# Optimization experiments

Hardware: AMD Instinct MI355X
Metric: run time of the kernel (lower is better)

Reference implementation:

```python
import jax, jax.numpy as jnp
import numpy as np

B, T, E, H = 4, 1024, 1024, 16
D = E // H  # head_dim = 64


def setup_inputs() -> dict:
    key = jax.random.key(0)
    ks = jax.random.split(key, 6)
    s = 0.02  # realistic init scale for stable softmax
    return {
        "hidden_states": jax.random.normal(ks[0], (B, T, E), jnp.float32),
        "attention_mask": jnp.zeros((B, 1, T, T), jnp.float32),
        "Wq": jax.random.normal(ks[1], (E, E), jnp.float32) * s,
        "bq": jnp.zeros((E,), jnp.float32),
        "Wk": jax.random.normal(ks[2], (E, E), jnp.float32) * s,
        "bk": jnp.zeros((E,), jnp.float32),
        "Wv": jax.random.normal(ks[3], (E, E), jnp.float32) * s,
        "bv": jnp.zeros((E,), jnp.float32),
        "Wo": jax.random.normal(ks[4], (E, E), jnp.float32) * s,
        "bo": jnp.zeros((E,), jnp.float32),
    }


def reference(hidden_states, attention_mask, Wq, bq, Wk, bk, Wv, bv, Wo, bo):
    b, t, e = hidden_states.shape
    scaling = jnp.asarray(D, hidden_states.dtype) ** -0.5
    # q_proj weights/bias are pre-scaled in the module; equivalent to scaling q output
    q = (hidden_states @ Wq.T + bq) * scaling      # [B,T,E]
    k = hidden_states @ Wk.T + bk                   # self-attention path (no cache)
    v = hidden_states @ Wv.T + bv
    q = q.reshape(b, t, H, D)
    k = k.reshape(b, t, H, D)
    v = v.reshape(b, t, H, D)
    # bmm(q, k^T): [B,H,T,S] score matrix (materialized, as in the original)
    scores = jnp.einsum("bthd,bshd->bhts", q, k) + attention_mask
    probs = jax.nn.softmax(scores, axis=-1)
    ctx = jnp.einsum("bhts,bshd->bthd", probs, v).reshape(b, t, e)
    return ctx @ Wo.T + bo
```

## Files before the change

kernel.cpp:

```cpp
#include <hip/hip_runtime.h>
#include <math.h>

#define BB 4
#define TT 1024
#define EE 1024
#define HH 16
#define DD 64
#define KDIM 1024
#define N_HS (4096 * 1024)
#define N_W  (1024 * 1024)
#define NQKV (BB * HH * TT * DD)
#define NMASK (BB * TT * TT)

typedef _Float16 f16x8 __attribute__((ext_vector_type(8)));
typedef _Float16 f16x4 __attribute__((ext_vector_type(4)));
typedef float    f32x4 __attribute__((ext_vector_type(4)));

__device__ __forceinline__ unsigned short f2h(float x) {
    _Float16 h = (_Float16)x;
    return __builtin_bit_cast(unsigned short, h);
}
__device__ __forceinline__ void split_h(float x, unsigned short& hi, unsigned short& lo) {
    _Float16 h = (_Float16)x;
    hi = __builtin_bit_cast(unsigned short, h);
    lo = f2h(x - (float)h);
}

__device__ __forceinline__ void gload16(const void* g, void* l) {
    __builtin_amdgcn_global_load_lds(
        (const __attribute__((address_space(1))) void*)g,
        (__attribute__((address_space(3))) void*)l, 16, 0, 0);
}

__global__ __launch_bounds__(256)
void split_kernel(const float* __restrict__ hs,
                  const float* __restrict__ Wq, const float* __restrict__ Wk,
                  const float* __restrict__ Wv, const float* __restrict__ Wo,
                  const float* __restrict__ maskp,
                  unsigned short* __restrict__ ws,
                  unsigned short* __restrict__ maskh)
{
    const int u = blockIdx.x * 256 + threadIdx.x;
    const float* src;
    unsigned short* dst;
    if (u < (N_HS / 4)) {
        src = hs + (size_t)u * 4;
        dst = ws + (size_t)u * 4;
    } else if (u < (N_HS / 4) + N_W) {
        int v = u - N_HS / 4;
        int wsel = v >> 18;
        int wo   = v & 0x3FFFF;
        const float* Wsrc = (wsel == 0) ? Wq : (wsel == 1) ? Wk : (wsel == 2) ? Wv : Wo;
        src = Wsrc + (size_t)wo * 4;
        dst = ws + (size_t)N_HS + (size_t)wsel * N_W + (size_t)wo * 4;
    } else {
        int v = u - (N_HS / 4) - N_W;
        src = maskp + (size_t)v * 4;
        dst = maskh + (size_t)v * 4;
    }
    float4 x = *(const float4*)src;
    ushort4 h4;
    h4.x = f2h(x.x); h4.y = f2h(x.y); h4.z = f2h(x.z); h4.w = f2h(x.w);
    *(ushort4*)dst = h4;
}

__global__ __launch_bounds__(256)
void qkv_kernel(const unsigned short* __restrict__ hsp,
                const unsigned short* __restrict__ wqp,
                const float* __restrict__ bq, const float* __restrict__ bk,
                const float* __restrict__ bv,
                unsigned short* __restrict__ qkvb)
{
    __shared__ unsigned short Ah[128 * 32], Bh[128 * 32];

    const int widx  = blockIdx.x >> 3;
    const int nbase = (blockIdx.x & 7) * 128;
    const int mbase = blockIdx.y * 128;
    const unsigned short* Wp = wqp + (size_t)widx * N_W;
    const float* bias = (widx == 0) ? bq : (widx == 1) ? bk : bv;
    unsigned short* dst = qkvb + (size_t)widx * NQKV;
    const float scale = (widx == 0) ? 0.125f : 1.0f;

    const int tid  = threadIdx.x;
    const int w    = tid >> 6;
    const int lane = tid & 63;
    const int quad = lane >> 4;
    const int l16  = lane & 15;
    const int wm   = (w >> 1) * 64;
    const int wn   = (w & 1) * 64;

    f32x4 acc[4][4];
#pragma unroll
    for (int i = 0; i < 4; i++)
#pragma unroll
        for (int j = 0; j < 4; j++) acc[i][j] = (f32x4)0.f;

#pragma unroll 1
    for (int kt = 0; kt < KDIM; kt += 32) {
        __syncthreads();
#pragma unroll
        for (int i = 0; i < 2; i++) {
            int u = tid + i * 256;
            int r = u >> 2, c = u & 3;
            int q = c ^ ((r >> 1) & 3);
            gload16(hsp + (size_t)(mbase + r) * KDIM + kt + q * 8, &Ah[u * 8]);
            gload16(Wp  + (size_t)(nbase + r) * KDIM + kt + q * 8, &Bh[u * 8]);
        }
        __syncthreads();

        f16x8 af[4], bfr[4];
#pragma unroll
        for (int i = 0; i < 4; i++) {
            int r = wm + i * 16 + l16;
            af[i] = *(const f16x8*)&Ah[(r * 4 + (quad ^ ((r >> 1) & 3))) * 8];
        }
#pragma unroll
        for (int j = 0; j < 4; j++) {
            int r = wn + j * 16 + l16;
            bfr[j] = *(const f16x8*)&Bh[(r * 4 + (quad ^ ((r >> 1) & 3))) * 8];
        }
#pragma unroll
        for (int i = 0; i < 4; i++)
#pragma unroll
            for (int j = 0; j < 4; j++)
                acc[i][j] = __builtin_amdgcn_mfma_f32_16x16x32_f16(af[i], bfr[j], acc[i][j], 0, 0, 0);
    }

#pragma unroll
    for (int j = 0; j < 4; j++) {
        int n = nbase + wn + j * 16 + l16;
        int h = n >> 6, d = n & 63;
        float bj = bias[n];
#pragma unroll
        for (int i = 0; i < 4; i++)
#pragma unroll
            for (int rr = 0; rr < 4; rr++) {
                int m = mbase + wm + i * 16 + quad * 4 + rr;
                int b = m >> 10, t = m & 1023;
                dst[(((size_t)(b * HH + h) * TT + t) * DD + d)] =
                    f2h((acc[i][j][rr] + bj) * scale);
            }
    }
}

__global__ __launch_bounds__(256)
void vtrans_kernel(const unsigned short* __restrict__ vp,
                   unsigned short* __restrict__ vtp)
{
    __shared__ unsigned short Ts[64 * 72];
    const int bh = blockIdx.y;
    const int t0 = blockIdx.x * 64;
    const unsigned short* src = vp  + (size_t)bh * TT * DD + (size_t)t0 * DD;
    unsigned short*       dst = vtp + (size_t)bh * DD * TT + t0;
    const int tid = threadIdx.x;

#pragma unroll
    for (int i = 0; i < 2; i++) {
        int id = tid + i * 256;
        int r = id >> 3, c = id & 7;
        *(uint4*)&Ts[r * 72 + c * 8] = *(const uint4*)(src + (size_t)r * DD + c * 8);
    }
    __syncthreads();
#pragma unroll
    for (int i = 0; i < 2; i++) {
        int id = tid + i * 256;
        int d = id >> 3, c = id & 7;
        unsigned short tmp[8];
#pragma unroll
        for (int j = 0; j < 8; j++) tmp[j] = Ts[(c * 8 + j) * 72 + d];
        uint4 o;
        o.x = (unsigned int)tmp[0] | ((unsigned int)tmp[1] << 16);
        o.y = (unsigned int)tmp[2] | ((unsigned int)tmp[3] << 16);
        o.z = (unsigned int)tmp[4] | ((unsigned int)tmp[5] << 16);
        o.w = (unsigned int)tmp[6] | ((unsigned int)tmp[7] << 16);
        *(uint4*)(dst + (size_t)d * TT + c * 8) = o;
    }
}

__global__ __launch_bounds__(256)
void outproj_kernel(const unsigned short* __restrict__ ctxh,
                    const unsigned short* __restrict__ ctxl,
                    const unsigned short* __restrict__ wop,
                    const float* __restrict__ bo, float* __restrict__ out)
{
    __shared__ unsigned short Ach[64 * 32], Acl[64 * 32], Bh[128 * 32];

    const int nbase = blockIdx.x * 128;
    const int mbase = blockIdx.y * 64;

    const int tid  = threadIdx.x;
    const int w    = tid >> 6;
    const int lane = tid & 63;
    const int quad = lane >> 4;
    const int l16  = lane & 15;
    const int wm   = (w >> 1) * 32;
    const int wn   = (w & 1) * 64;

    f32x4 acc[2][4];
#pragma unroll
    for (int i = 0; i < 2; i++)
#pragma unroll
        for (int j = 0; j < 4; j++) acc[i][j] = (f32x4)0.f;

#pragma unroll 1
    for (int kt = 0; kt < KDIM; kt += 32) {
        __syncthreads();
        {
            int r = tid >> 2, c = tid & 3;
            int q = c ^ ((r >> 1) & 3);
            size_t ga = (size_t)(mbase + r) * KDIM + kt + q * 8;
            gload16(ctxh + ga, &Ach[tid * 8]);
            gload16(ctxl + ga, &Acl[tid * 8]);
        }
#pragma unroll
        for (int i = 0; i < 2; i++) {
            int u = tid + i * 256;
            int r = u >> 2, c = u & 3;
            int q = c ^ ((r >> 1) & 3);
            gload16(wop + (size_t)(nbase + r) * KDIM + kt + q * 8, &Bh[u * 8]);
        }
        __syncthreads();

        f16x8 ah[2], al[2], bfr[4];
#pragma unroll
        for (int i = 0; i < 2; i++) {
            int r = wm + i * 16 + l16;
            int slot = (r * 4 + (quad ^ ((r >> 1) & 3))) * 8;
            ah[i] = *(const f16x8*)&Ach[slot];
            al[i] = *(const f16x8*)&Acl[slot];
        }
#pragma unroll
        for (int j = 0; j < 4; j++) {
            int r = wn + j * 16 + l16;
            bfr[j] = *(const f16x8*)&Bh[(r * 4 + (quad ^ ((r >> 1) & 3))) * 8];
        }
#pragma unroll
        for (int i = 0; i < 2; i++)
#pragma unroll
            for (int j = 0; j < 4; j++) {
                acc[i][j] = __builtin_amdgcn_mfma_f32_16x16x32_f16(ah[i], bfr[j], acc[i][j], 0, 0, 0);
                acc[i][j] = __builtin_amdgcn_mfma_f32_16x16x32_f16(al[i], bfr[j], acc[i][j], 0, 0, 0);
            }
    }

#pragma unroll
    for (int j = 0; j < 4; j++) {
        int n = nbase + wn + j * 16 + l16;
        float bj = bo[n];
#pragma unroll
        for (int i = 0; i < 2; i++)
#pragma unroll
            for (int rr = 0; rr < 4; rr++) {
                int m = mbase + wm + i * 16 + quad * 4 + rr;
                out[(size_t)m * EE + n] = acc[i][j][rr] + bj;
            }
    }
}

__global__ __launch_bounds__(128)
void attn_kernel(const unsigned short* __restrict__ qp_, const unsigned short* __restrict__ kp_,
                 const unsigned short* __restrict__ vtp_,
                 const unsigned short* __restrict__ maskh,
                 unsigned short* __restrict__ ctxh, unsigned short* __restrict__ ctxl)
{
    __shared__ unsigned short Ks[64 * 64];
    __shared__ unsigned short Vt[64 * 64];
    __shared__ unsigned short Ms[32 * 72];

    const int bh = blockIdx.x;
    const int b  = bh >> 4;
    const int h  = bh & 15;
    const int m0 = blockIdx.y * 32;
    const size_t hoff = (size_t)bh * TT * DD;
    const unsigned short* qhp = qp_ + hoff;
    const unsigned short* khp = kp_ + hoff;
    const unsigned short* vtp = vtp_ + hoff;
    const unsigned short* mb  = maskh + (size_t)b * TT * TT;

    const int tid  = threadIdx.x;
    const int w    = tid >> 6;
    const int lane = tid & 63;
    const int quad = lane >> 4;
    const int l16  = lane & 15;

    f16x8 qf[2];
#pragma unroll
    for (int s = 0; s < 2; s++)
        qf[s] = *(const f16x8*)(qhp + (size_t)(m0 + w * 16 + l16) * DD + s * 32 + quad * 8);

    f32x4 o[4];
#pragma unroll
    for (int u = 0; u < 4; u++) o[u] = (f32x4)0.f;
    float m_run = -INFINITY, lacc = 0.f;

#pragma unroll 1
    for (int n0 = 0; n0 < TT; n0 += 64) {
        __syncthreads();
#pragma unroll
        for (int i = 0; i < 4; i++) {
            int u = tid + i * 128;
            int r = u >> 3, cp = u & 7;
            int c = cp ^ (r & 7);
            gload16(khp + (size_t)(n0 + r) * DD + c * 8, &Ks[u * 8]);
            gload16(vtp + (size_t)r * TT + n0 + c * 8,   &Vt[u * 8]);
        }
#pragma unroll
        for (int i = 0; i < 2; i++) {
            int cch = tid * 2 + i;
            int row = cch >> 3, c8 = cch & 7;
            uint4 mv = *(const uint4*)(mb + (size_t)(m0 + row) * TT + n0 + c8 * 8);
            *(uint4*)&Ms[row * 72 + c8 * 8] = mv;
        }
        __syncthreads();

        f32x4 st[4];
#pragma unroll
        for (int t = 0; t < 4; t++) st[t] = (f32x4)0.f;
#pragma unroll
        for (int s = 0; s < 2; s++)
#pragma unroll
            for (int t = 0; t < 4; t++) {
                int R = 16 * t + l16;
                const f16x8 kf = *(const f16x8*)&Ks[(R * 8 + ((s * 4 + quad) ^ (R & 7))) * 8];
                st[t] = __builtin_amdgcn_mfma_f32_16x16x32_f16(kf, qf[s], st[t], 0, 0, 0);
            }
#pragma unroll
        for (int t = 0; t < 4; t++) {
            f16x4 mk = *(const f16x4*)&Ms[(w * 16 + l16) * 72 + 16 * t + quad * 4];
#pragma unroll
            for (int r = 0; r < 4; r++)
                st[t][r] += (float)mk[r];
        }

        float rm = st[0][0];
#pragma unroll
        for (int t = 0; t < 4; t++)
#pragma unroll
            for (int r = 0; r < 4; r++) rm = fmaxf(rm, st[t][r]);
        rm = fmaxf(rm, __shfl_xor(rm, 16));
        rm = fmaxf(rm, __shfl_xor(rm, 32));
        float mnew  = fmaxf(m_run, rm);
        float alpha = __expf(m_run - mnew);
        m_run = mnew;

        float ls = 0.f;
#pragma unroll
        for (int t = 0; t < 4; t++)
#pragma unroll
            for (int r = 0; r < 4; r++) {
                float p = __expf(st[t][r] - m_run);
                st[t][r] = p;
                ls += p;
            }
        lacc = lacc * alpha + ls;
#pragma unroll
        for (int u = 0; u < 4; u++)
#pragma unroll
            for (int r = 0; r < 4; r++)
                o[u][r] *= alpha;

        f16x4 pf[4];
#pragma unroll
        for (int t = 0; t < 4; t++)
#pragma unroll
            for (int r = 0; r < 4; r++)
                pf[t][r] = (_Float16)st[t][r];

#pragma unroll
        for (int t = 0; t < 4; t++)
#pragma unroll
            for (int u = 0; u < 4; u++) {
                int r_ = 16 * u + l16;
                int lc = 2 * t + (quad >> 1);
                int pc = lc ^ (r_ & 7);
                const f16x4 vf = *(const f16x4*)&Vt[r_ * 64 + pc * 8 + (quad & 1) * 4];
                o[u] = __builtin_amdgcn_mfma_f32_16x16x16f16(vf, pf[t], o[u], 0, 0, 0);
            }
    }

    lacc += __shfl_xor(lacc, 16);
    lacc += __shfl_xor(lacc, 32);
    const float inv = 1.0f / lacc;

    __syncthreads();
#pragma unroll
    for (int u = 0; u < 4; u++)
#pragma unroll
        for (int r = 0; r < 4; r++) {
            float val = o[u][r] * inv;
            unsigned short hi, lo;
            split_h(val, hi, lo);
            int mloc = w * 16 + l16;
            int d    = 16 * u + quad * 4 + r;
            Ks[mloc * 72 + d] = hi;
            Vt[mloc * 72 + d] = lo;
        }
    __syncthreads();
    {
        int row = tid >> 2;
        int c16 = (tid & 3) * 16;
        size_t base = ((size_t)(b * TT + m0 + row)) * EE + h * DD + c16;
        uint4 h0 = *(const uint4*)&Ks[row * 72 + c16];
        uint4 h1 = *(const uint4*)&Ks[row * 72 + c16 + 8];
        *(uint4*)(ctxh + base)     = h0;
        *(uint4*)(ctxh + base + 8) = h1;
        uint4 l0 = *(const uint4*)&Vt[row * 72 + c16];
        uint4 l1 = *(const uint4*)&Vt[row * 72 + c16 + 8];
        *(uint4*)(ctxl + base)     = l0;
        *(uint4*)(ctxl + base + 8) = l1;
    }
}

extern "C" void kernel_launch(void* const* d_in, const int* in_sizes, int n_in,
                              void* d_out, int out_size, void* d_ws, size_t ws_size,
                              hipStream_t stream)
{
    const float* hs   = (const float*)d_in[0];
    const float* mask = (const float*)d_in[1];
    const float* Wq   = (const float*)d_in[2];
    const float* bq   = (const float*)d_in[3];
    const float* Wk   = (const float*)d_in[4];
    const float* bk   = (const float*)d_in[5];
    const float* Wv   = (const float*)d_in[6];
    const float* bv   = (const float*)d_in[7];
    const float* Wo   = (const float*)d_in[8];
    const float* bo   = (const float*)d_in[9];
    float* out = (float*)d_out;

    unsigned short* ws    = (unsigned short*)d_ws;
    unsigned short* hsp   = ws;
    unsigned short* wqp   = ws + (size_t)N_HS;
    unsigned short* wop   = wqp + 3 * (size_t)N_W;
    unsigned short* qkvb  = wqp + 4 * (size_t)N_W;
    unsigned short* qp    = qkvb;
    unsigned short* kp    = qp + (size_t)NQKV;
    unsigned short* vp    = kp + (size_t)NQKV;
    unsigned short* vtp   = vp + (size_t)NQKV;
    unsigned short* ctxl  = vtp + (size_t)NQKV;
    unsigned short* maskh = ctxl + (size_t)N_HS;
    unsigned short* ctxh  = ws;

    split_kernel<<<12288, 256, 0, stream>>>(hs, Wq, Wk, Wv, Wo, mask, ws, maskh);
    qkv_kernel<<<dim3(24, 32), 256, 0, stream>>>(hsp, wqp, bq, bk, bv, qkvb);
    vtrans_kernel<<<dim3(TT / 64, BB * HH), 256, 0, stream>>>(vp, vtp);
    attn_kernel<<<dim3(BB * HH, TT / 32), 128, 0, stream>>>(qp, kp, vtp, maskh, ctxh, ctxl);
    outproj_kernel<<<dim3(8, 64), 256, 0, stream>>>(ctxh, ctxl, wop, bo, out);
}
```

Measured before the change: 235.6 us.

## Drop hi/lo ctx split, use 16x16x32 MFMA for PV via LDS-staged probabilities

The attention context is now written as a single fp16 tensor instead of a hi/lo pair, so the output projection does half the A-side loads and MFMAs. In the attention kernel, probabilities are staged through shared memory and the P·V product switches from 16x16x16 to 16x16x32 MFMAs using the swizzled V tile. Mask values are loaded straight into registers rather than copied through shared memory, and the final store goes directly from registers. This gives up the extra precision of the compensated split, and the direct ctx store writes only one 2-byte element per lane per row.

```diff
diff --git a/kernel.cpp b/kernel.cpp
--- a/kernel.cpp
+++ b/kernel.cpp
@@ -19,11 +19,6 @@
 __device__ __forceinline__ unsigned short f2h(float x) {
     _Float16 h = (_Float16)x;
     return __builtin_bit_cast(unsigned short, h);
-}
-__device__ __forceinline__ void split_h(float x, unsigned short& hi, unsigned short& lo) {
-    _Float16 h = (_Float16)x;
-    hi = __builtin_bit_cast(unsigned short, h);
-    lo = f2h(x - (float)h);
 }
 
 __device__ __forceinline__ void gload16(const void* g, void* l) {
@@ -179,11 +174,10 @@
 
 __global__ __launch_bounds__(256)
 void outproj_kernel(const unsigned short* __restrict__ ctxh,
-                    const unsigned short* __restrict__ ctxl,
                     const unsigned short* __restrict__ wop,
                     const float* __restrict__ bo, float* __restrict__ out)
 {
-    __shared__ unsigned short Ach[64 * 32], Acl[64 * 32], Bh[128 * 32];
+    __shared__ unsigned short Ach[64 * 32], Bh[128 * 32];
 
     const int nbase = blockIdx.x * 128;
     const int mbase = blockIdx.y * 64;
@@ -208,9 +202,7 @@
         {
             int r = tid >> 2, c = tid & 3;
             int q = c ^ ((r >> 1) & 3);
-            size_t ga = (size_t)(mbase + r) * KDIM + kt + q * 8;
-            gload16(ctxh + ga, &Ach[tid * 8]);
-            gload16(ctxl + ga, &Acl[tid * 8]);
+            gload16(ctxh + (size_t)(mbase + r) * KDIM + kt + q * 8, &Ach[tid * 8]);
         }
 #pragma unroll
         for (int i = 0; i < 2; i++) {
@@ -221,13 +213,11 @@
         }
         __syncthreads();
 
-        f16x8 ah[2], al[2], bfr[4];
+        f16x8 ah[2], bfr[4];
 #pragma unroll
         for (int i = 0; i < 2; i++) {
             int r = wm + i * 16 + l16;
-            int slot = (r * 4 + (quad ^ ((r >> 1) & 3))) * 8;
-            ah[i] = *(const f16x8*)&Ach[slot];
-            al[i] = *(const f16x8*)&Acl[slot];
+            ah[i] = *(const f16x8*)&Ach[(r * 4 + (quad ^ ((r >> 1) & 3))) * 8];
         }
 #pragma unroll
         for (int j = 0; j < 4; j++) {
@@ -237,10 +227,8 @@
 #pragma unroll
         for (int i = 0; i < 2; i++)
 #pragma unroll
-            for (int j = 0; j < 4; j++) {
+            for (int j = 0; j < 4; j++)
                 acc[i][j] = __builtin_amdgcn_mfma_f32_16x16x32_f16(ah[i], bfr[j], acc[i][j], 0, 0, 0);
-                acc[i][j] = __builtin_amdgcn_mfma_f32_16x16x32_f16(al[i], bfr[j], acc[i][j], 0, 0, 0);
-            }
     }
 
 #pragma unroll
@@ -261,11 +249,11 @@
 void attn_kernel(const unsigned short* __restrict__ qp_, const unsigned short* __restrict__ kp_,
                  const unsigned short* __restrict__ vtp_,
                  const unsigned short* __restrict__ maskh,
-                 unsigned short* __restrict__ ctxh, unsigned short* __restrict__ ctxl)
+                 unsigned short* __restrict__ ctxh)
 {
     __shared__ unsigned short Ks[64 * 64];
     __shared__ unsigned short Vt[64 * 64];
-    __shared__ unsigned short Ms[32 * 72];
+    __shared__ unsigned short Ps[32 * 72];
 
     const int bh = blockIdx.x;
     const int b  = bh >> 4;
@@ -275,26 +263,32 @@
     const unsigned short* qhp = qp_ + hoff;
     const unsigned short* khp = kp_ + hoff;
     const unsigned short* vtp = vtp_ + hoff;
-    const unsigned short* mb  = maskh + (size_t)b * TT * TT;
+    const _Float16* mb = (const _Float16*)(maskh + (size_t)b * TT * TT);
 
     const int tid  = threadIdx.x;
     const int w    = tid >> 6;
     const int lane = tid & 63;
     const int quad = lane >> 4;
     const int l16  = lane & 15;
+    const int mrow = m0 + w * 16 + l16;
 
     f16x8 qf[2];
 #pragma unroll
     for (int s = 0; s < 2; s++)
-        qf[s] = *(const f16x8*)(qhp + (size_t)(m0 + w * 16 + l16) * DD + s * 32 + quad * 8);
+        qf[s] = *(const f16x8*)(qhp + (size_t)mrow * DD + s * 32 + quad * 8);
 
     f32x4 o[4];
 #pragma unroll
-    for (int u = 0; u < 4; u++) o[u] = (f32x4)0.f;
+    for (int v = 0; v < 4; v++) o[v] = (f32x4)0.f;
     float m_run = -INFINITY, lacc = 0.f;
 
 #pragma unroll 1
     for (int n0 = 0; n0 < TT; n0 += 64) {
+        f16x4 mk[4];
+#pragma unroll
+        for (int t = 0; t < 4; t++)
+            mk[t] = *(const f16x4*)(mb + (size_t)mrow * TT + n0 + 16 * t + quad * 4);
+
         __syncthreads();
 #pragma unroll
         for (int i = 0; i < 4; i++) {
@@ -304,13 +298,6 @@
             gload16(khp + (size_t)(n0 + r) * DD + c * 8, &Ks[u * 8]);
             gload16(vtp + (size_t)r * TT + n0 + c * 8,   &Vt[u * 8]);
         }
-#pragma unroll
-        for (int i = 0; i < 2; i++) {
-            int cch = tid * 2 + i;
-            int row = cch >> 3, c8 = cch & 7;
-            uint4 mv = *(const uint4*)(mb + (size_t)(m0 + row) * TT + n0 + c8 * 8);
-            *(uint4*)&Ms[row * 72 + c8 * 8] = mv;
-        }
         __syncthreads();
 
         f32x4 st[4];
@@ -325,12 +312,10 @@
                 st[t] = __builtin_amdgcn_mfma_f32_16x16x32_f16(kf, qf[s], st[t], 0, 0, 0);
             }
 #pragma unroll
-        for (int t = 0; t < 4; t++) {
-            f16x4 mk = *(const f16x4*)&Ms[(w * 16 + l16) * 72 + 16 * t + quad * 4];
+        for (int t = 0; t < 4; t++)
 #pragma unroll
             for (int r = 0; r < 4; r++)
-                st[t][r] += (float)mk[r];
-        }
+                st[t][r] += (float)mk[t][r];
 
         float rm = st[0][0];
 #pragma unroll
@@ -353,61 +338,50 @@
                 ls += p;
             }
         lacc = lacc * alpha + ls;
-#pragma unroll
-        for (int u = 0; u < 4; u++)
+
+        float ar[4];
+#pragma unroll
+        for (int r = 0; r < 4; r++) ar[r] = __shfl(alpha, quad * 4 + r);
+#pragma unroll
+        for (int v = 0; v < 4; v++)
 #pragma unroll
             for (int r = 0; r < 4; r++)
-                o[u][r] *= alpha;
-
-        f16x4 pf[4];
-#pragma unroll
-        for (int t = 0; t < 4; t++)
-#pragma unroll
-            for (int r = 0; r < 4; r++)
-                pf[t][r] = (_Float16)st[t][r];
-
-#pragma unroll
-        for (int t = 0; t < 4; t++)
-#pragma unroll
-            for (int u = 0; u < 4; u++) {
-                int r_ = 16 * u + l16;
-                int lc = 2 * t + (quad >> 1);
-                int pc = lc ^ (r_ & 7);
-                const f16x4 vf = *(const f16x4*)&Vt[r_ * 64 + pc * 8 + (quad & 1) * 4];
-                o[u] = __builtin_amdgcn_mfma_f32_16x16x16f16(vf, pf[t], o[u], 0, 0, 0);
+                o[v][r] *= ar[r];
+
+#pragma unroll
+        for (int t = 0; t < 4; t++) {
+            f16x4 pk;
+#pragma unroll
+            for (int r = 0; r < 4; r++) pk[r] = (_Float16)st[t][r];
+            *(f16x4*)&Ps[(w * 16 + l16) * 72 + 16 * t + quad * 4] = pk;
+        }
+
+#pragma unroll
+        for (int s = 0; s < 2; s++) {
+            const f16x8 pf = *(const f16x8*)&Ps[(w * 16 + l16) * 72 + s * 32 + quad * 8];
+#pragma unroll
+            for (int v = 0; v < 4; v++) {
+                int R = 16 * v + l16;
+                const f16x8 vf = *(const f16x8*)&Vt[(R * 8 + ((s * 4 + quad) ^ (R & 7))) * 8];
+                o[v] = __builtin_amdgcn_mfma_f32_16x16x32_f16(pf, vf, o[v], 0, 0, 0);
             }
+        }
     }
 
     lacc += __shfl_xor(lacc, 16);
     lacc += __shfl_xor(lacc, 32);
-    const float inv = 1.0f / lacc;
-
-    __syncthreads();
-#pragma unroll
-    for (int u = 0; u < 4; u++)
-#pragma unroll
-        for (int r = 0; r < 4; r++) {
-            float val = o[u][r] * inv;
-            unsigned short hi, lo;
-            split_h(val, hi, lo);
-            int mloc = w * 16 + l16;
-            int d    = 16 * u + quad * 4 + r;
-            Ks[mloc * 72 + d] = hi;
-            Vt[mloc * 72 + d] = lo;
-        }
-    __syncthreads();
-    {
-        int row = tid >> 2;
-        int c16 = (tid & 3) * 16;
-        size_t base = ((size_t)(b * TT + m0 + row)) * EE + h * DD + c16;
-        uint4 h0 = *(const uint4*)&Ks[row * 72 + c16];
-        uint4 h1 = *(const uint4*)&Ks[row * 72 + c16 + 8];
-        *(uint4*)(ctxh + base)     = h0;
-        *(uint4*)(ctxh + base + 8) = h1;
-        uint4 l0 = *(const uint4*)&Vt[row * 72 + c16];
-        uint4 l1 = *(const uint4*)&Vt[row * 72 + c16 + 8];
-        *(uint4*)(ctxl + base)     = l0;
-        *(uint4*)(ctxl + base + 8) = l1;
+    float linv = 1.0f / lacc;
+    float invr[4];
+#pragma unroll
+    for (int r = 0; r < 4; r++) invr[r] = __shfl(linv, quad * 4 + r);
+
+#pragma unroll
+    for (int r = 0; r < 4; r++) {
+        int m = m0 + w * 16 + quad * 4 + r;
+        size_t base = (size_t)(b * TT + m) * EE + h * DD;
+#pragma unroll
+        for (int v = 0; v < 4; v++)
+            ctxh[base + 16 * v + l16] = f2h(o[v][r] * invr[r]);
     }
 }
 
@@ -436,13 +410,12 @@
     unsigned short* kp    = qp + (size_t)NQKV;
     unsigned short* vp    = kp + (size_t)NQKV;
     unsigned short* vtp   = vp + (size_t)NQKV;
-    unsigned short* ctxl  = vtp + (size_t)NQKV;
-    unsigned short* maskh = ctxl + (size_t)N_HS;
+    unsigned short* maskh = vtp + (size_t)NQKV;
     unsigned short* ctxh  = ws;
 
     split_kernel<<<12288, 256, 0, stream>>>(hs, Wq, Wk, Wv, Wo, mask, ws, maskh);
     qkv_kernel<<<dim3(24, 32), 256, 0, stream>>>(hsp, wqp, bq, bk, bv, qkvb);
     vtrans_kernel<<<dim3(TT / 64, BB * HH), 256, 0, stream>>>(vp, vtp);
-    attn_kernel<<<dim3(BB * HH, TT / 32), 128, 0, stream>>>(qp, kp, vtp, maskh, ctxh, ctxl);
-    outproj_kernel<<<dim3(8, 64), 256, 0, stream>>>(ctxh, ctxl, wop, bo, out);
-}
+    attn_kernel<<<dim3(BB * HH, TT / 32), 128, 0, stream>>>(qp, kp, vtp, maskh, ctxh);
+    outproj_kernel<<<dim3(8, 64), 256, 0, stream>>>(ctxh, wop, bo, out);
+}
```

New measurement: 230.0 us. -2.4%, faster.
